# Optimization experiments

Hardware: AMD Instinct MI355X
Metric: run time of the kernel (lower is better)

The kernel has to match this reference:

```python
import jax, jax.numpy as jnp
import numpy as np

N = 100000   # nodes
E = 800000   # edges
D = 128      # input feature dim
H = 128      # hidden_channels
O = 64       # out_channels
L = 3        # num_layers
DROP_P = 0.5
NEG_SLOPE = 0.01  # F.leaky_relu default


def setup_inputs() -> dict:
    key = jax.random.key(0)
    ks = jax.random.split(key, 8)
    x = jax.random.normal(ks[0], (N, D), dtype=jnp.float32)
    edge_index = jax.random.randint(ks[1], (2, E), 0, N, dtype=jnp.int64)
    s = 1.0 / np.sqrt(D)
    Wl = jax.random.uniform(ks[2], (L, H, D), jnp.float32, -s, s)
    Wr = jax.random.uniform(ks[3], (L, H, D), jnp.float32, -s, s)
    b = jax.random.uniform(ks[4], (L, H), jnp.float32, -s, s)
    so = 1.0 / np.sqrt(H)
    Wo = jax.random.uniform(ks[5], (O, H), jnp.float32, -so, so)
    bo = jax.random.uniform(ks[6], (O,), jnp.float32, -so, so)
    return {"x": x, "edge_index": edge_index, "Wl": Wl, "Wr": Wr, "b": b, "Wo": Wo, "bo": bo}


def reference(x, edge_index, Wl, Wr, b, Wo, bo):
    src, dst = edge_index[0], edge_index[1]
    # in-degree counts for mean aggregation (computed once; graph is static)
    deg = jax.ops.segment_sum(jnp.ones((E,), x.dtype), dst, num_segments=N)
    inv_deg = jnp.where(deg > 0, 1.0 / jnp.maximum(deg, 1.0), 0.0)[:, None]  # [N,1]
    dkey = jax.random.key(42)
    for l in range(L):
        # SAGEConv: mean over incoming neighbor features, then two linears
        agg = jax.ops.segment_sum(x[src], dst, num_segments=N) * inv_deg  # [N,H]
        x = agg @ Wl[l].T + x @ Wr[l].T + b[l]
        x = jax.nn.leaky_relu(x, NEG_SLOPE)
        # dropout p=0.5 (training mode in torch F.dropout default); fixed keys
        keep = jax.random.bernoulli(jax.random.fold_in(dkey, l), 1.0 - DROP_P, x.shape)
        x = jnp.where(keep, x / (1.0 - DROP_P), 0.0)
    return x @ Wo.T + bo
```

## Files before the change

### kernel.cpp

```cpp
#include <hip/hip_runtime.h>
#include <cstdint>
#include <cstddef>

#define NN 100000
#define EE 800000
#define HD 128
#define OD 64
#define CAP 64
#define WPL 400000

typedef __attribute__((ext_vector_type(8))) short s16x8;
typedef __attribute__((ext_vector_type(4))) float f32x4;
typedef __attribute__((ext_vector_type(8))) unsigned short u16x8;

__device__ __forceinline__ unsigned short f2bf(float f) {
  unsigned u = __float_as_uint(f);
  return (unsigned short)((u + 0x7FFFu + ((u >> 16) & 1u)) >> 16);
}
__device__ __forceinline__ float bf2f(unsigned short v) {
  return __uint_as_float(((unsigned)v) << 16);
}

__host__ __device__ __forceinline__ unsigned rotl32(unsigned x, int r) {
#ifdef __HIP_DEVICE_COMPILE__
  return __builtin_amdgcn_alignbit(x, x, 32 - r);
#else
  return (x << r) | (x >> (32 - r));
#endif
}

__host__ __device__ __forceinline__ void tf2x32(unsigned k0, unsigned k1,
                                                unsigned x0, unsigned x1,
                                                unsigned& o0, unsigned& o1) {
  unsigned ks2 = k0 ^ k1 ^ 0x1BD11BDAu;
#define TFR(r) { x0 += x1; x1 = rotl32(x1, (r)) ^ x0; }
  x0 += k0; x1 += k1;
  TFR(13) TFR(15) TFR(26) TFR(6)
  x0 += k1; x1 += ks2 + 1u;
  TFR(17) TFR(29) TFR(16) TFR(24)
  x0 += ks2; x1 += k0 + 2u;
  TFR(13) TFR(15) TFR(26) TFR(6)
  x0 += k0; x1 += k1 + 3u;
  TFR(17) TFR(29) TFR(16) TFR(24)
  x0 += k1; x1 += ks2 + 4u;
  TFR(13) TFR(15) TFR(26) TFR(6)
  x0 += ks2; x1 += k0 + 5u;
#undef TFR
  o0 = x0; o1 = x1;
}

__device__ __forceinline__ void gen_mask_1024(unsigned long long* __restrict__ maskW,
                                              int wave, int lane,
                                              unsigned k0, unsigned k1) {
  const unsigned base = (unsigned)wave * 1024u + (unsigned)lane;
#pragma unroll
  for (int c = 0; c < 16; ++c) {
    unsigned r0, r1;
    tf2x32(k0, k1, 0u, base + (unsigned)(c << 6), r0, r1);
    unsigned long long m = __ballot(((r0 ^ r1) & 0x80000000u) == 0u);
    if (lane == 0) maskW[wave * 16 + c] = m;
  }
}

__device__ __forceinline__ void cast8(const float* __restrict__ x,
                                      unsigned short* __restrict__ xb, int t) {
  const float4* p = (const float4*)x + (size_t)t * 2;
  float4 v0 = p[0], v1 = p[1];
  u16x8 r;
  r[0] = f2bf(v0.x); r[1] = f2bf(v0.y); r[2] = f2bf(v0.z); r[3] = f2bf(v0.w);
  r[4] = f2bf(v1.x); r[5] = f2bf(v1.y); r[6] = f2bf(v1.z); r[7] = f2bf(v1.w);
  *((u16x8*)xb + t) = r;
}

__global__ __launch_bounds__(256) void k_castw(const float* __restrict__ Wl,
                                               const float* __restrict__ Wr,
                                               const float* __restrict__ Wo,
                                               unsigned short* __restrict__ Wb,
                                               unsigned short* __restrict__ Wob) {
  int t = blockIdx.x * 256 + threadIdx.x;
  if (t < 3 * 128 * 256) {
    int l = t >> 15;
    int rem = t & 32767;
    int n = rem >> 8;
    int k = rem & 255;
    float w = (k < 128) ? Wl[(l << 14) + (n << 7) + k] : Wr[(l << 14) + (n << 7) + (k - 128)];
    int sw = rem ^ ((n & 7) << 3);
    Wb[(l << 15) + sw] = f2bf(w);
  } else {
    int t3 = t - 3 * 128 * 256;
    if (t3 < OD * 128) Wob[t3] = f2bf(Wo[t3]);
  }
}

__global__ __launch_bounds__(256) void k_fill2(const int* __restrict__ ei,
                                               int* __restrict__ fill,
                                               int* __restrict__ bucket,
                                               unsigned long long* __restrict__ mask1,
                                               unsigned mk0, unsigned mk1,
                                               const float* __restrict__ x,
                                               unsigned short* __restrict__ xb) {
  const int e = blockIdx.x * 256 + threadIdx.x;
  unsigned s = (unsigned)ei[e];
  unsigned d = (unsigned)ei[EE + e];
  if (s >= NN) s = 0;
  if (d >= NN) d = 0;
  cast8(x, xb, e);
  cast8(x, xb, EE + e);
  gen_mask_1024(mask1, e >> 6, e & 63, mk0, mk1);
  int p = atomicAdd(&fill[d], 1);
  if (p < CAP) bucket[d * CAP + p] = (int)s;
}

__global__ __launch_bounds__(256) void k_aggb(const unsigned short* __restrict__ xb,
                                              const int* __restrict__ bucket,
                                              const int* __restrict__ fill,
                                              unsigned short* __restrict__ aggb,
                                              unsigned long long* __restrict__ maskW,
                                              unsigned mk0, unsigned mk1) {
  const int w = (blockIdx.x * 256 + threadIdx.x) >> 6;
  const int lane = threadIdx.x & 63;
  const int q = lane >> 4;
  const int ql = lane & 15;
  const int qb = q << 4;
  const int n = (w << 2) + q;

  const int degf = fill[n];
  const int deg = (degf < CAP) ? degf : CAP;
  int idx = (ql < deg) ? bucket[n * CAP + ql] : 0;
  const float sc = (degf > 0) ? 1.0f / (float)degf : 0.0f;

  if (maskW) {
    const unsigned base = (unsigned)w * 512u + (unsigned)lane;
#pragma unroll
    for (int c = 0; c < 8; ++c) {
      unsigned r0, r1;
      tf2x32(mk0, mk1, 0u, base + (unsigned)(c << 6), r0, r1);
      unsigned long long m = __ballot(((r0 ^ r1) & 0x80000000u) == 0u);
      if (lane == 0) maskW[(w << 3) + c] = m;
    }
  }

  const u16x8* xb8 = (const u16x8*)xb;
  float a0[8], a1[8], a2[8], a3[8];
#pragma unroll
  for (int k = 0; k < 8; ++k) { a0[k] = 0.f; a1[k] = 0.f; a2[k] = 0.f; a3[k] = 0.f; }

  const int dcap = (deg < 16) ? deg : 16;
  int i0 = 0;
  for (; i0 + 4 <= dcap; i0 += 4) {
    int j0 = __shfl(idx, qb + i0);
    int j1 = __shfl(idx, qb + i0 + 1);
    int j2 = __shfl(idx, qb + i0 + 2);
    int j3 = __shfl(idx, qb + i0 + 3);
    u16x8 v0 = xb8[(size_t)j0 * 16 + ql];
    u16x8 v1 = xb8[(size_t)j1 * 16 + ql];
    u16x8 v2 = xb8[(size_t)j2 * 16 + ql];
    u16x8 v3 = xb8[(size_t)j3 * 16 + ql];
#pragma unroll
    for (int k = 0; k < 8; ++k) {
      a0[k] += bf2f(v0[k]); a1[k] += bf2f(v1[k]);
      a2[k] += bf2f(v2[k]); a3[k] += bf2f(v3[k]);
    }
  }
  {
    const int rem = dcap - i0;
    int j0 = __shfl(idx, qb + (i0 & 15));
    int j1 = __shfl(idx, qb + ((i0 + 1) & 15));
    int j2 = __shfl(idx, qb + ((i0 + 2) & 15));
    if (rem > 0) {
      u16x8 v = xb8[(size_t)j0 * 16 + ql];
#pragma unroll
      for (int k = 0; k < 8; ++k) a0[k] += bf2f(v[k]);
    }
    if (rem > 1) {
      u16x8 v = xb8[(size_t)j1 * 16 + ql];
#pragma unroll
      for (int k = 0; k < 8; ++k) a1[k] += bf2f(v[k]);
    }
    if (rem > 2) {
      u16x8 v = xb8[(size_t)j2 * 16 + ql];
#pragma unroll
      for (int k = 0; k < 8; ++k) a2[k] += bf2f(v[k]);
    }
  }
  for (int i = 16; i < deg; ++i) {
    int sX = bucket[n * CAP + i];
    u16x8 v = xb8[(size_t)sX * 16 + ql];
#pragma unroll
    for (int k = 0; k < 8; ++k) a3[k] += bf2f(v[k]);
  }

  u16x8 o;
#pragma unroll
  for (int k = 0; k < 8; ++k)
    o[k] = f2bf(((a0[k] + a1[k]) + (a2[k] + a3[k])) * sc);
  ((u16x8*)aggb)[(size_t)n * 16 + ql] = o;
}

__global__ __launch_bounds__(256) void k_layer_mfma(
    const unsigned short* __restrict__ xin,
    const unsigned short* __restrict__ aggb,
    const unsigned short* __restrict__ Wb,
    const float* __restrict__ bias,
    const unsigned* __restrict__ mask,
    unsigned short* __restrict__ xout) {
  __shared__ unsigned short Wlds[16384];
  const int tid = threadIdx.x;
  const int lane = tid & 63;
  const int wv = tid >> 6;
  const int rbase = blockIdx.x * 64 + wv * 16;
  const int lr = lane & 15;
  const int lkq = lane >> 4;
  const int rowg = lkq * 4;

  const f32x4* Wv = (const f32x4*)Wb;
  f32x4* dst = (f32x4*)Wlds;

  f32x4 acc[8];
#pragma unroll
  for (int j = 0; j < 8; ++j) acc[j] = (f32x4){0.f, 0.f, 0.f, 0.f};

  int n0 = rbase + lr;
  if (n0 >= NN) n0 = NN - 1;

  const char* WL = (const char*)Wlds;
#pragma unroll
  for (int half = 0; half < 2; ++half) {
    if (half) __syncthreads();
#pragma unroll
    for (int it = 0; it < 8; ++it) {
      const int c = it * 256 + tid;
      dst[c] = Wv[((c >> 4) << 5) + (half << 4) + (c & 15)];
    }
    __syncthreads();
    const unsigned short* A = half ? xin : aggb;
#pragma unroll
    for (int kfl = 0; kfl < 4; ++kfl) {
      const int kc = kfl * 32 + lkq * 8;
      s16x8 a0 = *(const s16x8*)(A + (size_t)n0 * 128 + kc);
#pragma unroll
      for (int nf = 0; nf < 8; ++nf) {
        const int row = nf * 16 + lr;
        const int bo = (row << 8) + ((((kfl << 6) + (lkq << 4)) ^ ((row & 7) << 4)));
        s16x8 wfr = *(const s16x8*)(WL + bo);
        acc[nf] = __builtin_amdgcn_mfma_f32_16x16x32_bf16(wfr, a0, acc[nf], 0, 0, 0);
      }
    }
  }

  const int node = rbase + lr;
  if (node < NN) {
    const unsigned mbase = (unsigned)node * 4u;
#pragma unroll
    for (int nf = 0; nf < 8; ++nf) {
      const int colb = nf * 16 + rowg;
      const float4 bv = *(const float4*)(bias + colb);
      const unsigned mw = mask[mbase + (colb >> 5)];
      const unsigned sh = (unsigned)(colb & 31);
      float v0 = acc[nf][0] + bv.x;
      float v1 = acc[nf][1] + bv.y;
      float v2 = acc[nf][2] + bv.z;
      float v3 = acc[nf][3] + bv.w;
      v0 = (v0 > 0.f) ? v0 : 0.01f * v0;
      v1 = (v1 > 0.f) ? v1 : 0.01f * v1;
      v2 = (v2 > 0.f) ? v2 : 0.01f * v2;
      v3 = (v3 > 0.f) ? v3 : 0.01f * v3;
      ushort4 o;
      o.x = ((mw >> (sh + 0)) & 1u) ? f2bf(v0 + v0) : (unsigned short)0;
      o.y = ((mw >> (sh + 1)) & 1u) ? f2bf(v1 + v1) : (unsigned short)0;
      o.z = ((mw >> (sh + 2)) & 1u) ? f2bf(v2 + v2) : (unsigned short)0;
      o.w = ((mw >> (sh + 3)) & 1u) ? f2bf(v3 + v3) : (unsigned short)0;
      *(ushort4*)(xout + (size_t)node * 128 + colb) = o;
    }
  }
}

__global__ __launch_bounds__(256) void k_final_mfma(
    const unsigned short* __restrict__ xin,
    const unsigned short* __restrict__ Wob,
    const float* __restrict__ bo,
    float* __restrict__ out) {
  const int lane = threadIdx.x & 63;
  const int wv = threadIdx.x >> 6;
  const int rbase = blockIdx.x * 64 + wv * 16;
  const int lr = lane & 15;
  const int lk = (lane >> 4) * 8;
  const int rowg = (lane >> 4) * 4;

  f32x4 acc[4];
#pragma unroll
  for (int j = 0; j < 4; ++j) acc[j] = (f32x4){0.f, 0.f, 0.f, 0.f};

  int n0 = rbase + lr;
  if (n0 >= NN) n0 = NN - 1;

#pragma unroll
  for (int kf = 0; kf < 4; ++kf) {
    const int kc = kf * 32 + lk;
    s16x8 act0 = *(const s16x8*)(xin + (size_t)n0 * 128 + kc);
#pragma unroll
    for (int nf = 0; nf < 4; ++nf) {
      s16x8 wfr = *(const s16x8*)(Wob + (nf * 16 + lr) * 128 + kc);
      acc[nf] = __builtin_amdgcn_mfma_f32_16x16x32_bf16(wfr, act0, acc[nf], 0, 0, 0);
    }
  }

  const int node = rbase + lr;
  if (node < NN) {
#pragma unroll
    for (int nf = 0; nf < 4; ++nf) {
      const int colb = nf * 16 + rowg;
      const float4 bv = *(const float4*)(bo + colb);
      float4 o;
      o.x = acc[nf][0] + bv.x;
      o.y = acc[nf][1] + bv.y;
      o.z = acc[nf][2] + bv.z;
      o.w = acc[nf][3] + bv.w;
      *(float4*)(out + (size_t)node * 64 + colb) = o;
    }
  }
}

extern "C" void kernel_launch(void* const* d_in, const int* in_sizes, int n_in,
                              void* d_out, int out_size, void* d_ws, size_t ws_size,
                              hipStream_t stream) {
  const float* x  = (const float*)d_in[0];
  const int*   ei = (const int*)d_in[1];
  const float* Wl = (const float*)d_in[2];
  const float* Wr = (const float*)d_in[3];
  const float* b  = (const float*)d_in[4];
  const float* Wo = (const float*)d_in[5];
  const float* bo = (const float*)d_in[6];
  float* out = (float*)d_out;

  char* wsp = (char*)d_ws;
  size_t off = 0;
  auto take = [&](size_t bytes) -> void* {
    off = (off + 255) & ~(size_t)255;
    void* p = wsp + off;
    off += bytes;
    return p;
  };
  unsigned short* xb0    = (unsigned short*)take((size_t)NN * 128 * 2);
  unsigned short* act1   = (unsigned short*)take((size_t)NN * 128 * 2);
  unsigned short* act2   = (unsigned short*)take((size_t)NN * 128 * 2);
  unsigned short* aggb   = (unsigned short*)take((size_t)NN * 128 * 2);
  unsigned short* Wb     = (unsigned short*)take((size_t)3 * 128 * 256 * 2);
  unsigned short* Wob    = (unsigned short*)take((size_t)OD * 128 * 2);
  unsigned*       masks  = (unsigned*)take((size_t)3 * WPL * 4);
  int*            bucket = (int*)take((size_t)NN * CAP * 4);
  int*            fill   = (int*)take((size_t)NN * 4);

  unsigned fk[3][2];
  for (int l = 0; l < 3; ++l) tf2x32(0u, 42u, 0u, (unsigned)l, fk[l][0], fk[l][1]);

  hipMemsetAsync(fill, 0, (size_t)NN * 4, stream);
  k_castw<<<(3 * 128 * 256 + OD * 128 + 255) / 256, 256, 0, stream>>>(Wl, Wr, Wo, Wb, Wob);
  k_fill2<<<EE / 256, 256, 0, stream>>>(ei, fill, bucket,
                                        (unsigned long long*)(masks + WPL),
                                        fk[1][0], fk[1][1], x, xb0);

  const int gemmBlocks = (NN + 63) / 64;
  const int aggBlocks  = 6250;

  k_aggb<<<aggBlocks, 256, 0, stream>>>(xb0, bucket, fill, aggb,
                                        (unsigned long long*)masks, fk[0][0], fk[0][1]);
  k_layer_mfma<<<gemmBlocks, 256, 0, stream>>>(xb0, aggb, Wb, b, masks, act1);

  k_aggb<<<aggBlocks, 256, 0, stream>>>(act1, bucket, fill, aggb,
                                        (unsigned long long*)(masks + 2 * WPL),
                                        fk[2][0], fk[2][1]);
  k_layer_mfma<<<gemmBlocks, 256, 0, stream>>>(act1, aggb, Wb + 32768, b + 128,
                                               masks + WPL, act2);

  k_aggb<<<aggBlocks, 256, 0, stream>>>(act2, bucket, fill, aggb,
                                        (unsigned long long*)0, 0u, 0u);
  k_layer_mfma<<<gemmBlocks, 256, 0, stream>>>(act2, aggb, Wb + 65536, b + 256,
                                               masks + 2 * WPL, act1);

  k_final_mfma<<<gemmBlocks, 256, 0, stream>>>(act1, Wob, bo, out);

  (void)in_sizes; (void)n_in; (void)out_size; (void)ws_size;
}
```

Before: 291.7 us.

## Fuse third SAGE layer with output projection through shared memory

Merges the last layer's MFMA GEMM (with bias, leaky ReLU and dropout) and the final output linear into one kernel. The layer-3 activations are staged in LDS instead of being written to and re-read from global memory, which also removes one launch. The weights are staged into a swizzled LDS layout in two halves, which adds block-level syncs. It also moves the atomicAdd in the fill kernel earlier so its latency can overlap with the cast and mask work.

```diff
diff --git a/kernel.cpp b/kernel.cpp
--- a/kernel.cpp
+++ b/kernel.cpp
@@ -8,6 +8,7 @@
 #define OD 64
 #define CAP 64
 #define WPL 400000
+#define ALDS 136
 
 typedef __attribute__((ext_vector_type(8))) short s16x8;
 typedef __attribute__((ext_vector_type(4))) float f32x4;
@@ -104,10 +105,10 @@
   unsigned d = (unsigned)ei[EE + e];
   if (s >= NN) s = 0;
   if (d >= NN) d = 0;
+  int p = atomicAdd(&fill[d], 1);
   cast8(x, xb, e);
   cast8(x, xb, EE + e);
   gen_mask_1024(mask1, e >> 6, e & 63, mk0, mk1);
-  int p = atomicAdd(&fill[d], 1);
   if (p < CAP) bucket[d * CAP + p] = (int)s;
 }
 
@@ -275,33 +276,102 @@
   }
 }
 
-__global__ __launch_bounds__(256) void k_final_mfma(
+__global__ __launch_bounds__(256) void k_layer3_final(
     const unsigned short* __restrict__ xin,
+    const unsigned short* __restrict__ aggb,
+    const unsigned short* __restrict__ Wb,
+    const float* __restrict__ bias,
+    const unsigned* __restrict__ mask,
     const unsigned short* __restrict__ Wob,
     const float* __restrict__ bo,
     float* __restrict__ out) {
-  const int lane = threadIdx.x & 63;
-  const int wv = threadIdx.x >> 6;
+  __shared__ unsigned short smem[16384];
+  const int tid = threadIdx.x;
+  const int lane = tid & 63;
+  const int wv = tid >> 6;
   const int rbase = blockIdx.x * 64 + wv * 16;
   const int lr = lane & 15;
-  const int lk = (lane >> 4) * 8;
-  const int rowg = (lane >> 4) * 4;
-
-  f32x4 acc[4];
-#pragma unroll
-  for (int j = 0; j < 4; ++j) acc[j] = (f32x4){0.f, 0.f, 0.f, 0.f};
+  const int lkq = lane >> 4;
+  const int rowg = lkq * 4;
+
+  const f32x4* Wv = (const f32x4*)Wb;
+  f32x4* dst = (f32x4*)smem;
+
+  f32x4 acc[8];
+#pragma unroll
+  for (int j = 0; j < 8; ++j) acc[j] = (f32x4){0.f, 0.f, 0.f, 0.f};
 
   int n0 = rbase + lr;
   if (n0 >= NN) n0 = NN - 1;
 
+  const char* WL = (const char*)smem;
+#pragma unroll
+  for (int half = 0; half < 2; ++half) {
+    if (half) __syncthreads();
+#pragma unroll
+    for (int it = 0; it < 8; ++it) {
+      const int c = it * 256 + tid;
+      dst[c] = Wv[((c >> 4) << 5) + (half << 4) + (c & 15)];
+    }
+    __syncthreads();
+    const unsigned short* A = half ? xin : aggb;
+#pragma unroll
+    for (int kfl = 0; kfl < 4; ++kfl) {
+      const int kc = kfl * 32 + lkq * 8;
+      s16x8 a0 = *(const s16x8*)(A + (size_t)n0 * 128 + kc);
+#pragma unroll
+      for (int nf = 0; nf < 8; ++nf) {
+        const int row = nf * 16 + lr;
+        const int bo2 = (row << 8) + ((((kfl << 6) + (lkq << 4)) ^ ((row & 7) << 4)));
+        s16x8 wfr = *(const s16x8*)(WL + bo2);
+        acc[nf] = __builtin_amdgcn_mfma_f32_16x16x32_bf16(wfr, a0, acc[nf], 0, 0, 0);
+      }
+    }
+  }
+
+  __syncthreads();
+  {
+    const int node = rbase + lr;
+    const int nodec = (node < NN) ? node : (NN - 1);
+    const unsigned mbase = (unsigned)nodec * 4u;
+    const int arow = wv * 16 + lr;
+#pragma unroll
+    for (int nf = 0; nf < 8; ++nf) {
+      const int colb = nf * 16 + rowg;
+      const float4 bv = *(const float4*)(bias + colb);
+      const unsigned mw = mask[mbase + (colb >> 5)];
+      const unsigned sh = (unsigned)(colb & 31);
+      float v0 = acc[nf][0] + bv.x;
+      float v1 = acc[nf][1] + bv.y;
+      float v2 = acc[nf][2] + bv.z;
+      float v3 = acc[nf][3] + bv.w;
+      v0 = (v0 > 0.f) ? v0 : 0.01f * v0;
+      v1 = (v1 > 0.f) ? v1 : 0.01f * v1;
+      v2 = (v2 > 0.f) ? v2 : 0.01f * v2;
+      v3 = (v3 > 0.f) ? v3 : 0.01f * v3;
+      ushort4 o;
+      o.x = ((mw >> (sh + 0)) & 1u) ? f2bf(v0 + v0) : (unsigned short)0;
+      o.y = ((mw >> (sh + 1)) & 1u) ? f2bf(v1 + v1) : (unsigned short)0;
+      o.z = ((mw >> (sh + 2)) & 1u) ? f2bf(v2 + v2) : (unsigned short)0;
+      o.w = ((mw >> (sh + 3)) & 1u) ? f2bf(v3 + v3) : (unsigned short)0;
+      *(ushort4*)(smem + arow * ALDS + colb) = o;
+    }
+  }
+  __syncthreads();
+
+  f32x4 acc2[4];
+#pragma unroll
+  for (int j = 0; j < 4; ++j) acc2[j] = (f32x4){0.f, 0.f, 0.f, 0.f};
+
+  const int arow = wv * 16 + lr;
 #pragma unroll
   for (int kf = 0; kf < 4; ++kf) {
-    const int kc = kf * 32 + lk;
-    s16x8 act0 = *(const s16x8*)(xin + (size_t)n0 * 128 + kc);
+    const int kc = kf * 32 + lkq * 8;
+    s16x8 a0 = *(const s16x8*)(smem + arow * ALDS + kc);
 #pragma unroll
     for (int nf = 0; nf < 4; ++nf) {
       s16x8 wfr = *(const s16x8*)(Wob + (nf * 16 + lr) * 128 + kc);
-      acc[nf] = __builtin_amdgcn_mfma_f32_16x16x32_bf16(wfr, act0, acc[nf], 0, 0, 0);
+      acc2[nf] = __builtin_amdgcn_mfma_f32_16x16x32_bf16(wfr, a0, acc2[nf], 0, 0, 0);
     }
   }
 
@@ -312,10 +382,10 @@
       const int colb = nf * 16 + rowg;
       const float4 bv = *(const float4*)(bo + colb);
       float4 o;
-      o.x = acc[nf][0] + bv.x;
-      o.y = acc[nf][1] + bv.y;
-      o.z = acc[nf][2] + bv.z;
-      o.w = acc[nf][3] + bv.w;
+      o.x = acc2[nf][0] + bv.x;
+      o.y = acc2[nf][1] + bv.y;
+      o.z = acc2[nf][2] + bv.z;
+      o.w = acc2[nf][3] + bv.w;
       *(float4*)(out + (size_t)node * 64 + colb) = o;
     }
   }
@@ -375,10 +445,8 @@
 
   k_aggb<<<aggBlocks, 256, 0, stream>>>(act2, bucket, fill, aggb,
                                         (unsigned long long*)0, 0u, 0u);
-  k_layer_mfma<<<gemmBlocks, 256, 0, stream>>>(act2, aggb, Wb + 65536, b + 256,
-                                               masks + 2 * WPL, act1);
-
-  k_final_mfma<<<gemmBlocks, 256, 0, stream>>>(act1, Wob, bo, out);
+  k_layer3_final<<<gemmBlocks, 256, 0, stream>>>(act2, aggb, Wb + 65536, b + 256,
+                                                 masks + 2 * WPL, Wob, bo, out);
 
   (void)in_sizes; (void)n_in; (void)out_size; (void)ws_size;
 }
```

New measurement: 272.9 us. 1.07x faster.
